# Kernel optimization log

Measured on AMD Instinct MI355X. Metric: run time of the kernel, lower is better.

## Reference

```python
import jax, jax.numpy as jnp
import numpy as np

B, L, D = 16, 4096, 512
WORD_SIZE = 2048  # codebook_size // 4
WORD_LEN = 2


def setup_inputs() -> dict:
    key = jax.random.key(0)
    k1, k2, k3, k4, k5 = jax.random.split(key, 5)
    char_tokens = jax.random.randint(k1, (B, L), 0, 8192, dtype=jnp.int64 if jax.config.jax_enable_x64 else jnp.int32)
    char_embeddings = jax.random.normal(k2, (B, L, D), dtype=jnp.float32)
    # word_codebook initialized uniform(-1/word_size, 1/word_size) in the original
    word_codebook = jax.random.uniform(k3, (WORD_SIZE, D), dtype=jnp.float32,
                                       minval=-1.0 / WORD_SIZE, maxval=1.0 / WORD_SIZE)
    proj_w = jax.random.normal(k4, (D, D), dtype=jnp.float32) * (1.0 / np.sqrt(D))
    proj_b = jax.random.normal(k5, (D,), dtype=jnp.float32) * 0.01
    return {"char_tokens": char_tokens, "char_embeddings": char_embeddings,
            "word_codebook": word_codebook, "proj_w": proj_w, "proj_b": proj_b}


def reference(char_tokens, char_embeddings, word_codebook, proj_w, proj_b):
    Bv, Lv, Dv = char_embeddings.shape
    G = Lv // WORD_LEN  # number of 2-char groups per sequence
    # mean-pool each consecutive pair of characters -> [B, G, D]
    means = char_embeddings.reshape(Bv, G, WORD_LEN, Dv).mean(axis=2)
    # squared-euclidean nearest codebook entry (same argmin as cdist)
    # d2[b,g,k] = ||m||^2 - 2 m.W^T + ||W||^2 ; ||m||^2 constant over k -> drop
    dots = jnp.einsum('bgd,kd->bgk', means, word_codebook)            # [B,G,K]
    cb_sq = jnp.sum(word_codebook * word_codebook, axis=-1)           # [K]
    word_indices = jnp.argmin(cb_sq[None, None, :] - 2.0 * dots, axis=-1)  # [B,G]
    word_embeddings = word_codebook[word_indices]                     # [B,G,D]
    # alignment loss: mse(proj(word_emb), stop_grad(word_emb))
    projected = jnp.einsum('bgd,ed->bge', word_embeddings, proj_w) + proj_b
    target = jax.lax.stop_gradient(word_embeddings)
    alignment_loss = jnp.mean((projected - target) ** 2)
    return (word_indices, word_embeddings, alignment_loss)
```

## Files before the change

### kernel.cpp

```cpp
#include <hip/hip_runtime.h>


#define D_DIM    512
#define K_CODES  2048
#define N_ROWS   32768
#define EPS_GAP  1e-5f
#define LOSS_SCALE (1.0f / 16777216.0f)

typedef __attribute__((ext_vector_type(8))) short short8;
typedef __attribute__((ext_vector_type(4))) float f32x4;

__device__ __forceinline__ void split_bf16(float f, unsigned short& h, unsigned short& l) {
    unsigned u = __float_as_uint(f);
    h = (unsigned short)(u >> 16);
    float hr = __uint_as_float(u & 0xFFFF0000u);
    l = (unsigned short)(__float_as_uint(f - hr) >> 16);
}

__device__ __forceinline__ void dma16(const void* g, void* l) {
    __builtin_amdgcn_global_load_lds(
        (const __attribute__((address_space(1))) unsigned int*)g,
        (__attribute__((address_space(3))) unsigned int*)l, 16, 0, 0);
}

__device__ __forceinline__ void merge_cand(float s, int idx, float& v1, int& i1, float& v2, int& i2) {
    if (s < v1 || (s == v1 && idx < i1)) { v2 = v1; i2 = i1; v1 = s; i1 = idx; }
    else if (s < v2 || (s == v2 && idx < i2)) { v2 = s; i2 = idx; }
}

__global__ __launch_bounds__(256, 1)
void cra_pack_a(const float* __restrict__ ce,
                unsigned short* __restrict__ Ap)
{
    const int tid = threadIdx.x;
    const int mb  = blockIdx.x;
    const int rq  = tid >> 5;
    const int dq  = tid & 31;
    const int dbase = dq * 16;
    const int ach = dq >> 1;
    const int k0  = (dq & 1) * 16;

    #pragma unroll 2
    for (int p = 0; p < 16; ++p) {
        const int r  = p * 8 + rq;
        const int gr = mb * 128 + r;
        const float* a0 = ce + (size_t)(2 * gr) * D_DIM + dbase;
        const float* a1 = a0 + D_DIM;
        float4 x0[4], x1[4];
        #pragma unroll
        for (int q = 0; q < 4; ++q) {
            x0[q] = *(const float4*)(a0 + q * 4);
            x1[q] = *(const float4*)(a1 + q * 4);
        }
        short8 h8[2], l8[2];
        #pragma unroll
        for (int q = 0; q < 4; ++q) {
            const float m[4] = {0.5f * (x0[q].x + x1[q].x), 0.5f * (x0[q].y + x1[q].y),
                                0.5f * (x0[q].z + x1[q].z), 0.5f * (x0[q].w + x1[q].w)};
            #pragma unroll
            for (int e = 0; e < 4; ++e) {
                unsigned short hh, ll;
                split_bf16(m[e], hh, ll);
                h8[q >> 1][(q & 1) * 4 + e] = (short)hh;
                l8[q >> 1][(q & 1) * 4 + e] = (short)ll;
            }
        }
        const size_t hb = ((size_t)(mb * 32 + ach) * 128 + r) * 32 + k0;
        const size_t lb = ((size_t)(mb * 32 + 16 + ach) * 128 + r) * 32 + k0;
        *(short8*)(Ap + hb)     = h8[0];
        *(short8*)(Ap + hb + 8) = h8[1];
        *(short8*)(Ap + lb)     = l8[0];
        *(short8*)(Ap + lb + 8) = l8[1];
    }
}

__global__ __launch_bounds__(256, 1)
void cra_pack_b(const float* __restrict__ cb,
                unsigned short* __restrict__ Bp,
                float* __restrict__ cb_sq,
                float* __restrict__ Sk,
                int* __restrict__ counter,
                float* __restrict__ loss_out)
{
    __shared__ float cbs[32 * D_DIM];
    const int tid = threadIdx.x;
    const int c0  = blockIdx.x * 32;

    if (blockIdx.x == 0) {
        #pragma unroll
        for (int j = 0; j < 8; ++j) Sk[tid + j * 256] = 0.0f;
        if (tid == 0) { counter[0] = 0; loss_out[0] = 0.0f; }
    }

    {
        const float4* src = (const float4*)(cb + (size_t)c0 * D_DIM);
        float4* dst = (float4*)cbs;
        #pragma unroll
        for (int k = 0; k < 16; ++k) dst[tid + k * 256] = src[tid + k * 256];
    }
    __syncthreads();

    if (tid < 32) {
        const float* r = cbs + tid * D_DIM;
        float s = 0.f;
        for (int d = 0; d < D_DIM; ++d) s = fmaf(r[d], r[d], s);
        cb_sq[c0 + tid] = s;
    }

    const int row  = tid >> 3;
    const int k    = c0 + row;
    const int colb = k >> 7;
    const int pr   = k & 127;
    const int dspan = (tid & 7) * 64;
    #pragma unroll
    for (int g = 0; g < 8; ++g) {
        const int d   = dspan + g * 8;
        const int bch = d >> 5;
        const int k0  = d & 31;
        short8 h8, l8;
        #pragma unroll
        for (int e = 0; e < 8; ++e) {
            unsigned short hh, ll;
            split_bf16(cbs[row * D_DIM + d + e], hh, ll);
            h8[e] = (short)hh; l8[e] = (short)ll;
        }
        *(short8*)(Bp + ((size_t)(colb * 32 + bch) * 128 + pr) * 32 + k0)      = h8;
        *(short8*)(Bp + ((size_t)(colb * 32 + 16 + bch) * 128 + pr) * 32 + k0) = l8;
    }
}

__global__ __launch_bounds__(256, 1)
void cra_proj(const float* __restrict__ cb,
              const float* __restrict__ W,
              const float* __restrict__ pb,
              float* __restrict__ Sk)
{
    __shared__ float cbs[32 * D_DIM];
    __shared__ float red[4 * 32];
    const int tid = threadIdx.x;
    const int cblock = blockIdx.x >> 2;
    const int eb     = blockIdx.x & 3;
    const int c0 = cblock * 32;

    {
        const float4* src = (const float4*)(cb + (size_t)c0 * D_DIM);
        float4* dst = (float4*)cbs;
        #pragma unroll
        for (int k = 0; k < 16; ++k) dst[tid + k * 256] = src[tid + k * 256];
    }
    __syncthreads();

    const int e  = eb * 128 + (tid >> 1);
    const int dh = (tid & 1) * 256;
    float acc[32];
    #pragma unroll
    for (int c = 0; c < 32; ++c) acc[c] = 0.f;
    const float4* wrow = (const float4*)(W + (size_t)e * D_DIM + dh);
    for (int dq = 0; dq < 64; ++dq) {
        const float4 wv = wrow[dq];
        #pragma unroll
        for (int c = 0; c < 32; ++c) {
            const float4 cv = *(const float4*)&cbs[c * D_DIM + dh + dq * 4];
            acc[c] += cv.x * wv.x + cv.y * wv.y + cv.z * wv.z + cv.w * wv.w;
        }
    }
    const float bias = pb[e];
    const int w = tid >> 6;
    #pragma unroll
    for (int c = 0; c < 32; ++c) {
        const float full = acc[c] + __shfl_xor(acc[c], 1);
        const float diff = full + bias - cbs[c * D_DIM + e];
        float v = (tid & 1) ? 0.f : diff * diff;
        #pragma unroll
        for (int off = 32; off > 0; off >>= 1) v += __shfl_down(v, off, 64);
        if ((tid & 63) == 0) red[w * 32 + c] = v;
    }
    __syncthreads();
    if (tid < 32)
        atomicAdd(&Sk[c0 + tid],
                  red[tid] + red[32 + tid] + red[64 + tid] + red[96 + tid]);
}

__global__ __launch_bounds__(256, 3)
void cra_gemm(const unsigned short* __restrict__ Ap,
              const unsigned short* __restrict__ Bp,
              const float* __restrict__ cb_sq,
              float4* __restrict__ wsRed)
{
    __shared__ short sMem[8192];
    short* sA = sMem;
    short* sB = sMem + 4096;

    const int tid  = threadIdx.x;
    const int bid  = blockIdx.x;
    const int xcd  = bid & 7;
    const int slot = bid >> 3;
    const int mb   = xcd * 32 + (slot >> 4);
    const int colb = slot & 15;
    const int rowBase = mb * 128;
    const int colBase = colb * 128;

    const int lane = tid & 63;
    const int w    = tid >> 6;
    const int wr   = (w & 1) * 64;
    const int wcH  = w >> 1;
    const int wc   = wcH * 64;
    const int cid  = lane & 15;
    const int quad = lane >> 4;

    f32x4 acc[4][4];
    #pragma unroll
    for (int i = 0; i < 4; ++i)
        #pragma unroll
        for (int j = 0; j < 4; ++j) acc[i][j] = (f32x4)(0.f);

    const char* Ag = (const char*)Ap + ((size_t)mb   * 32) * 8192 + w * 2048 + lane * 16;
    const char* Bg = (const char*)Bp + ((size_t)colb * 32) * 8192 + w * 2048 + lane * 16;
    char* lA = (char*)sA + w * 2048;
    char* lB = (char*)sB + w * 2048;

    #pragma unroll 1
    for (int g = 0; g < 48; ++g) {
        const int ach = g & 31;
        const int bch = (g & 15) | ((g & 32) >> 1);
        const char* ag = Ag + ach * 8192;
        const char* bg = Bg + bch * 8192;
        dma16(ag,        lA);
        dma16(ag + 1024, lA + 1024);
        dma16(bg,        lB);
        dma16(bg + 1024, lB + 1024);
        __syncthreads();

        short8 aF[4], bF[4];
        #pragma unroll
        for (int mi = 0; mi < 4; ++mi) aF[mi] = *(const short8*)&sA[(wr + mi * 16 + cid) * 32 + quad * 8];
        #pragma unroll
        for (int ni = 0; ni < 4; ++ni) bF[ni] = *(const short8*)&sB[(wc + ni * 16 + cid) * 32 + quad * 8];
        #pragma unroll
        for (int mi = 0; mi < 4; ++mi)
            #pragma unroll
            for (int ni = 0; ni < 4; ++ni)
                acc[mi][ni] = __builtin_amdgcn_mfma_f32_16x16x32_bf16(aF[mi], bF[ni], acc[mi][ni], 0, 0, 0);
        __syncthreads();
    }

    float cq[4];
    #pragma unroll
    for (int ni = 0; ni < 4; ++ni) cq[ni] = cb_sq[colBase + wc + ni * 16 + cid];

    float4* sRed = (float4*)sMem;
    #pragma unroll
    for (int mi = 0; mi < 4; ++mi) {
        #pragma unroll
        for (int reg = 0; reg < 4; ++reg) {
            float v1 = 3.4e38f, v2 = 3.4e38f;
            int   i1 = 0x7FFFFFFF, i2 = 0x7FFFFFFF;
            #pragma unroll
            for (int ni = 0; ni < 4; ++ni) {
                const float s = fmaf(-2.0f, acc[mi][ni][reg], cq[ni]);
                merge_cand(s, colBase + wc + ni * 16 + cid, v1, i1, v2, i2);
            }
            #pragma unroll
            for (int d = 1; d <= 2; d <<= 1) {
                float ov1 = __shfl_xor(v1, d); int oi1 = __shfl_xor(i1, d);
                float ov2 = __shfl_xor(v2, d); int oi2 = __shfl_xor(i2, d);
                merge_cand(ov1, oi1, v1, i1, v2, i2);
                merge_cand(ov2, oi2, v1, i1, v2, i2);
            }
            if ((cid & 3) == 0) {
                const int row = wr + mi * 16 + quad * 4 + reg;
                sRed[(row * 2 + wcH) * 4 + (cid >> 2)] =
                    make_float4(v1, __int_as_float(i1), v2, __int_as_float(i2));
            }
        }
    }
    __syncthreads();
    if (tid < 128) {
        float v1 = 3.4e38f, v2 = 3.4e38f;
        int   i1 = 0x7FFFFFFF, i2 = 0x7FFFFFFF;
        #pragma unroll
        for (int e = 0; e < 8; ++e) {
            const float4 t = sRed[tid * 8 + e];
            merge_cand(t.x, __float_as_int(t.y), v1, i1, v2, i2);
            merge_cand(t.z, __float_as_int(t.w), v1, i1, v2, i2);
        }
        wsRed[(size_t)(rowBase + tid) * 16 + colb] =
            make_float4(v1, __int_as_float(i1), v2, __int_as_float(i2));
    }
}

__global__ __launch_bounds__(256, 1)
void cra_merge(const float4* __restrict__ wsRed,
               const float* __restrict__ Sk,
               float* __restrict__ out_idx,
               float* __restrict__ out_loss,
               int* __restrict__ counter,
               int* __restrict__ flagRow,
               int2* __restrict__ flagI)
{
    __shared__ float sl[256];
    const int tid = threadIdx.x;
    const int r = blockIdx.x * 256 + tid;
    float v1 = 3.4e38f, v2 = 3.4e38f;
    int   i1 = 0x7FFFFFFF, i2 = 0x7FFFFFFF;
    #pragma unroll 4
    for (int cbk = 0; cbk < 16; ++cbk) {
        const float4 t = wsRed[(size_t)r * 16 + cbk];
        merge_cand(t.x, __float_as_int(t.y), v1, i1, v2, i2);
        merge_cand(t.z, __float_as_int(t.w), v1, i1, v2, i2);
    }
    out_idx[r] = (float)i1;
    if (v2 - v1 < EPS_GAP) {
        const int slot = atomicAdd(counter, 1);
        flagRow[slot] = r;
        flagI[slot] = make_int2(i1, i2);
    }
    sl[tid] = Sk[i1];
    __syncthreads();
    for (int s = 128; s > 0; s >>= 1) { if (tid < s) sl[tid] += sl[tid + s]; __syncthreads(); }
    if (tid == 0) atomicAdd(out_loss, sl[0] * LOSS_SCALE);
}

__global__ __launch_bounds__(256, 1)
void cra_gather(const float* __restrict__ out_idx,
                const float4* __restrict__ cb4,
                float4* __restrict__ out4)
{
    __shared__ int sidx[128];
    const int tid = threadIdx.x;
    const int rb = blockIdx.x * 128;
    if (tid < 128) sidx[tid] = (int)out_idx[rb + tid];
    __syncthreads();
    for (int j = tid; j < 128 * 128; j += 256) {
        const int row = j >> 7, q = j & 127;
        out4[(size_t)(rb + row) * 128 + q] = cb4[(size_t)sidx[row] * 128 + q];
    }
}

__global__ __launch_bounds__(256, 1)
void cra_recheck(const float* __restrict__ ce,
                 const float* __restrict__ cb,
                 const float* __restrict__ cb_sq,
                 const float* __restrict__ Sk,
                 const int* __restrict__ counter,
                 const int* __restrict__ flagRow,
                 const int2* __restrict__ flagI,
                 float* __restrict__ out_idx,
                 float4* __restrict__ out4,
                 float* __restrict__ out_loss,
                 const float4* __restrict__ cb4)
{
    __shared__ float rp[8];
    __shared__ int swin;
    const int tid = threadIdx.x;
    const int n = counter[0];
    for (int f = blockIdx.x; f < n; f += 64) {
        const int row = flagRow[f];
        const int2 ii = flagI[f];
        const int d0 = tid * 2;
        const float2 x0 = *(const float2*)(ce + (size_t)(2 * row) * D_DIM + d0);
        const float2 x1 = *(const float2*)(ce + (size_t)(2 * row) * D_DIM + D_DIM + d0);
        const float m0 = 0.5f * (x0.x + x1.x), m1 = 0.5f * (x0.y + x1.y);
        const float* c1 = cb + (size_t)ii.x * D_DIM + d0;
        const float* c2 = cb + (size_t)ii.y * D_DIM + d0;
        float p1 = fmaf(m0, c1[0], m1 * c1[1]);
        float p2 = fmaf(m0, c2[0], m1 * c2[1]);
        #pragma unroll
        for (int off = 32; off > 0; off >>= 1) {
            p1 += __shfl_down(p1, off, 64);
            p2 += __shfl_down(p2, off, 64);
        }
        if ((tid & 63) == 0) { rp[(tid >> 6) * 2] = p1; rp[(tid >> 6) * 2 + 1] = p2; }
        __syncthreads();
        if (tid == 0) {
            const float dot1 = rp[0] + rp[2] + rp[4] + rp[6];
            const float dot2 = rp[1] + rp[3] + rp[5] + rp[7];
            const float s1 = cb_sq[ii.x] - 2.f * dot1;
            const float s2 = cb_sq[ii.y] - 2.f * dot2;
            const int win = (s2 < s1 || (s2 == s1 && ii.y < ii.x)) ? ii.y : ii.x;
            swin = win;
            if (win != ii.x) {
                out_idx[row] = (float)win;
                atomicAdd(out_loss, (Sk[win] - Sk[ii.x]) * LOSS_SCALE);
            }
        }
        __syncthreads();
        if (swin != ii.x) {
            for (int q = tid; q < 128; q += 256)
                out4[(size_t)row * 128 + q] = cb4[(size_t)swin * 128 + q];
        }
        __syncthreads();
    }
}

extern "C" void kernel_launch(void* const* d_in, const int* in_sizes, int n_in,
                              void* d_out, int out_size, void* d_ws, size_t ws_size,
                              hipStream_t stream)
{
    const float* ce = (const float*)d_in[1];
    const float* cb = (const float*)d_in[2];
    const float* W  = (const float*)d_in[3];
    const float* pb = (const float*)d_in[4];

    char* ws = (char*)d_ws;
    unsigned short* Bp = (unsigned short*)ws;
    float4* wsRed  = (float4*)(ws + 4194304);
    float* cb_sq   = (float*)(ws + 12582912);
    float* Sk      = (float*)(ws + 12582912 + 8192);
    int*   flagRow = (int*)(ws + 12582912 + 16384);
    int2*  flagI   = (int2*)(ws + 12582912 + 16384 + 131072);
    int*   counter = (int*)(ws + 12582912 + 16384 + 131072 + 262144);

    float* out_idx  = (float*)d_out;
    float* out_emb  = out_idx + N_ROWS;
    float* out_loss = out_emb + (size_t)N_ROWS * D_DIM;
    unsigned short* Ap = (unsigned short*)out_emb;

    cra_pack_a<<<256, 256, 0, stream>>>(ce, Ap);
    cra_pack_b<<<64, 256, 0, stream>>>(cb, Bp, cb_sq, Sk, counter, out_loss);
    cra_proj<<<256, 256, 0, stream>>>(cb, W, pb, Sk);
    cra_gemm<<<4096, 256, 0, stream>>>(Ap, Bp, cb_sq, wsRed);
    cra_merge<<<128, 256, 0, stream>>>(wsRed, Sk, out_idx, out_loss, counter, flagRow, flagI);
    cra_gather<<<256, 256, 0, stream>>>(out_idx, (const float4*)cb, (float4*)out_emb);
    cra_recheck<<<64, 256, 0, stream>>>(ce, cb, cb_sq, Sk, counter, flagRow, flagI,
                                        out_idx, (float4*)out_emb, out_loss, (const float4*)cb);
}
```

Baseline: 867.0 us.

## Rework split-bf16 GEMM into 256x256 tiles with swizzled LDS and double-buffered DMA

Replaces the 128x128, 256-thread GEMM, which syncs twice per 32-wide K step, with a 512-thread 256x256 tile kernel. Each stage loads 64-wide K chunks into a 128KB LDS double buffer through direct global-to-LDS DMA, and explicit vmcnt waits let the next stage's loads overlap the current stage's MFMAs. The pack kernels now write A and B pre-swizzled (XOR pattern) so LDS fragment reads avoid bank conflicts, and the merge stage now combines 8 column partials per row instead of 16. The larger tiles raise data reuse per byte loaded but use much more LDS and registers, which lowers occupancy.

```diff
diff --git a/kernel.cpp b/kernel.cpp
--- a/kernel.cpp
+++ b/kernel.cpp
@@ -10,6 +10,8 @@
 typedef __attribute__((ext_vector_type(8))) short short8;
 typedef __attribute__((ext_vector_type(4))) float f32x4;
 
+#define SWZ(L) ((L) ^ (((L) >> 1) & 0x40) ^ (((L) >> 4) & 0x30))
+
 __device__ __forceinline__ void split_bf16(float f, unsigned short& h, unsigned short& l) {
     unsigned u = __float_as_uint(f);
     h = (unsigned short)(u >> 16);
@@ -32,19 +34,24 @@
 void cra_pack_a(const float* __restrict__ ce,
                 unsigned short* __restrict__ Ap)
 {
-    const int tid = threadIdx.x;
-    const int mb  = blockIdx.x;
-    const int rq  = tid >> 5;
-    const int dq  = tid & 31;
-    const int dbase = dq * 16;
-    const int ach = dq >> 1;
-    const int k0  = (dq & 1) * 16;
+    const int tid   = threadIdx.x;
+    const int mb128 = blockIdx.x;
+    const int mb256 = mb128 >> 1;
+    const int half  = mb128 & 1;
+    const int rq = tid >> 5;
+    const int dq = tid & 31;
+    const int d0 = dq * 16;
+    const int j  = dq >> 2;
+    const int k0 = (dq & 3) * 16;
+
+    const size_t hbase = ((size_t)((mb256 * 16 + j) * 2 + half)) * 8192;
+    const size_t lbase = ((size_t)((mb256 * 16 + 8 + j) * 2 + half)) * 8192;
 
     #pragma unroll 2
     for (int p = 0; p < 16; ++p) {
         const int r  = p * 8 + rq;
-        const int gr = mb * 128 + r;
-        const float* a0 = ce + (size_t)(2 * gr) * D_DIM + dbase;
+        const int gr = mb128 * 128 + r;
+        const float* a0 = ce + (size_t)(2 * gr) * D_DIM + d0;
         const float* a1 = a0 + D_DIM;
         float4 x0[4], x1[4];
         #pragma unroll
@@ -65,12 +72,13 @@
                 l8[q >> 1][(q & 1) * 4 + e] = (short)ll;
             }
         }
-        const size_t hb = ((size_t)(mb * 32 + ach) * 128 + r) * 32 + k0;
-        const size_t lb = ((size_t)(mb * 32 + 16 + ach) * 128 + r) * 32 + k0;
-        *(short8*)(Ap + hb)     = h8[0];
-        *(short8*)(Ap + hb + 8) = h8[1];
-        *(short8*)(Ap + lb)     = l8[0];
-        *(short8*)(Ap + lb + 8) = l8[1];
+        const int L1 = r * 128 + k0 * 2;
+        const int S1 = SWZ(L1);
+        const int S2 = SWZ(L1 + 16);
+        *(short8*)(Ap + hbase + (S1 >> 1)) = h8[0];
+        *(short8*)(Ap + hbase + (S2 >> 1)) = h8[1];
+        *(short8*)(Ap + lbase + (S1 >> 1)) = l8[0];
+        *(short8*)(Ap + lbase + (S2 >> 1)) = l8[1];
     }
 }
 
@@ -107,16 +115,18 @@
         cb_sq[c0 + tid] = s;
     }
 
-    const int row  = tid >> 3;
-    const int k    = c0 + row;
-    const int colb = k >> 7;
-    const int pr   = k & 127;
+    const int row   = tid >> 3;
+    const int k     = c0 + row;
+    const int colb  = k >> 8;
+    const int cc    = k & 255;
+    const int halfB = cc >> 7;
+    const int rB    = cc & 127;
     const int dspan = (tid & 7) * 64;
     #pragma unroll
     for (int g = 0; g < 8; ++g) {
-        const int d   = dspan + g * 8;
-        const int bch = d >> 5;
-        const int k0  = d & 31;
+        const int d  = dspan + g * 8;
+        const int j  = d >> 6;
+        const int kk = d & 63;
         short8 h8, l8;
         #pragma unroll
         for (int e = 0; e < 8; ++e) {
@@ -124,8 +134,9 @@
             split_bf16(cbs[row * D_DIM + d + e], hh, ll);
             h8[e] = (short)hh; l8[e] = (short)ll;
         }
-        *(short8*)(Bp + ((size_t)(colb * 32 + bch) * 128 + pr) * 32 + k0)      = h8;
-        *(short8*)(Bp + ((size_t)(colb * 32 + 16 + bch) * 128 + pr) * 32 + k0) = l8;
+        const int S = SWZ(rB * 128 + kk * 2);
+        *(short8*)(Bp + ((size_t)((colb * 16 + j) * 2 + halfB)) * 8192 + (S >> 1))     = h8;
+        *(short8*)(Bp + ((size_t)((colb * 16 + 8 + j) * 2 + halfB)) * 8192 + (S >> 1)) = l8;
     }
 }
 
@@ -181,76 +192,109 @@
                   red[tid] + red[32 + tid] + red[64 + tid] + red[96 + tid]);
 }
 
-__global__ __launch_bounds__(256, 3)
+__global__ __launch_bounds__(512, 2)
 void cra_gemm(const unsigned short* __restrict__ Ap,
               const unsigned short* __restrict__ Bp,
               const float* __restrict__ cb_sq,
               float4* __restrict__ wsRed)
 {
-    __shared__ short sMem[8192];
-    short* sA = sMem;
-    short* sB = sMem + 4096;
+    __shared__ __align__(16) char sMem[131072];
 
     const int tid  = threadIdx.x;
     const int bid  = blockIdx.x;
-    const int xcd  = bid & 7;
-    const int slot = bid >> 3;
-    const int mb   = xcd * 32 + (slot >> 4);
-    const int colb = slot & 15;
-    const int rowBase = mb * 128;
-    const int colBase = colb * 128;
+    const int wgid = (bid & 7) * 128 + (bid >> 3);
+    const int mb   = wgid >> 3;
+    const int colb = wgid & 7;
+    const int rowBase = mb * 256;
+    const int colBase = colb * 256;
 
     const int lane = tid & 63;
     const int w    = tid >> 6;
-    const int wr   = (w & 1) * 64;
-    const int wcH  = w >> 1;
-    const int wc   = wcH * 64;
+    const int wm   = w >> 2;
+    const int wn   = w & 3;
     const int cid  = lane & 15;
     const int quad = lane >> 4;
 
-    f32x4 acc[4][4];
-    #pragma unroll
-    for (int i = 0; i < 4; ++i)
-        #pragma unroll
-        for (int j = 0; j < 4; ++j) acc[i][j] = (f32x4)(0.f);
-
-    const char* Ag = (const char*)Ap + ((size_t)mb   * 32) * 8192 + w * 2048 + lane * 16;
-    const char* Bg = (const char*)Bp + ((size_t)colb * 32) * 8192 + w * 2048 + lane * 16;
-    char* lA = (char*)sA + w * 2048;
-    char* lB = (char*)sB + w * 2048;
+    const int swzm = ((cid & 1) << 6) | (((cid >> 1) & 3) << 4);
+    const int aRT  = (cid * 128 + quad * 16) ^ swzm;
+    const int bRT  = ((((wn & 1) * 64 + cid) * 128) + quad * 16) ^ swzm;
+
+    const char* AgBase = (const char*)Ap + (size_t)(mb * 16) * 32768 + w * 1024 + lane * 16;
+    const char* BgBase = (const char*)Bp + (size_t)(colb * 16) * 32768 + w * 1024 + lane * 16;
+
+    f32x4 acc[8][4];
+    #pragma unroll
+    for (int mi = 0; mi < 8; ++mi)
+        #pragma unroll
+        for (int ni = 0; ni < 4; ++ni) acc[mi][ni] = (f32x4)(0.f);
+
+    #pragma unroll
+    for (int p = 0; p < 2; ++p) {
+        const char* ag = AgBase + (size_t)p * 32768;
+        const char* bg = BgBase + (size_t)p * 32768;
+        char* la = sMem + p * 65536 + w * 1024;
+        char* lb = la + 32768;
+        #pragma unroll
+        for (int jj = 0; jj < 4; ++jj) {
+            dma16(ag + jj * 8192, la + jj * 8192);
+            dma16(bg + jj * 8192, lb + jj * 8192);
+        }
+    }
 
     #pragma unroll 1
-    for (int g = 0; g < 48; ++g) {
-        const int ach = g & 31;
-        const int bch = (g & 15) | ((g & 32) >> 1);
-        const char* ag = Ag + ach * 8192;
-        const char* bg = Bg + bch * 8192;
-        dma16(ag,        lA);
-        dma16(ag + 1024, lA + 1024);
-        dma16(bg,        lB);
-        dma16(bg + 1024, lB + 1024);
-        __syncthreads();
-
-        short8 aF[4], bF[4];
-        #pragma unroll
-        for (int mi = 0; mi < 4; ++mi) aF[mi] = *(const short8*)&sA[(wr + mi * 16 + cid) * 32 + quad * 8];
-        #pragma unroll
-        for (int ni = 0; ni < 4; ++ni) bF[ni] = *(const short8*)&sB[(wc + ni * 16 + cid) * 32 + quad * 8];
-        #pragma unroll
-        for (int mi = 0; mi < 4; ++mi)
+    for (int t = 0; t < 24; ++t) {
+        const int p = t & 1;
+        if (t < 23) asm volatile("s_waitcnt vmcnt(8)\n\ts_barrier" ::: "memory");
+        else        asm volatile("s_waitcnt vmcnt(0)\n\ts_barrier" ::: "memory");
+
+        const char* sAh = sMem + p * 65536 + wm * 16384;
+        const char* sBh = sMem + p * 65536 + 32768 + (wn >> 1) * 16384;
+
+        #pragma unroll
+        for (int ks = 0; ks < 2; ++ks) {
+            short8 af[8], bf[4];
+            #pragma unroll
+            for (int mi = 0; mi < 8; ++mi)
+                af[mi] = *(const short8*)(sAh + ((aRT ^ (ks << 6)) + mi * 2048));
             #pragma unroll
             for (int ni = 0; ni < 4; ++ni)
-                acc[mi][ni] = __builtin_amdgcn_mfma_f32_16x16x32_bf16(aF[mi], bF[ni], acc[mi][ni], 0, 0, 0);
-        __syncthreads();
-    }
+                bf[ni] = *(const short8*)(sBh + ((bRT ^ (ks << 6)) + ni * 2048));
+            __builtin_amdgcn_s_setprio(1);
+            #pragma unroll
+            for (int mi = 0; mi < 8; ++mi)
+                #pragma unroll
+                for (int ni = 0; ni < 4; ++ni)
+                    acc[mi][ni] = __builtin_amdgcn_mfma_f32_16x16x32_bf16(af[mi], bf[ni], acc[mi][ni], 0, 0, 0);
+            __builtin_amdgcn_s_setprio(0);
+        }
+
+        asm volatile("s_waitcnt lgkmcnt(0)\n\ts_barrier" ::: "memory");
+
+        if (t + 2 < 24) {
+            const int tn = t + 2;
+            const int at = tn < 16 ? tn : tn - 16;
+            const int bt = tn < 8 ? tn : tn - 8;
+            const char* ag = AgBase + (size_t)at * 32768;
+            const char* bg = BgBase + (size_t)bt * 32768;
+            char* la = sMem + p * 65536 + w * 1024;
+            char* lb = la + 32768;
+            #pragma unroll
+            for (int jj = 0; jj < 4; ++jj) {
+                dma16(ag + jj * 8192, la + jj * 8192);
+                dma16(bg + jj * 8192, lb + jj * 8192);
+            }
+        }
+    }
+
+    __syncthreads();
+    float4* sRed = (float4*)sMem;
 
     float cq[4];
     #pragma unroll
-    for (int ni = 0; ni < 4; ++ni) cq[ni] = cb_sq[colBase + wc + ni * 16 + cid];
-
-    float4* sRed = (float4*)sMem;
-    #pragma unroll
-    for (int mi = 0; mi < 4; ++mi) {
+    for (int ni = 0; ni < 4; ++ni) cq[ni] = cb_sq[colBase + wn * 64 + ni * 16 + cid];
+
+    #pragma unroll
+    for (int mi = 0; mi < 8; ++mi) {
         #pragma unroll
         for (int reg = 0; reg < 4; ++reg) {
             float v1 = 3.4e38f, v2 = 3.4e38f;
@@ -258,7 +302,7 @@
             #pragma unroll
             for (int ni = 0; ni < 4; ++ni) {
                 const float s = fmaf(-2.0f, acc[mi][ni][reg], cq[ni]);
-                merge_cand(s, colBase + wc + ni * 16 + cid, v1, i1, v2, i2);
+                merge_cand(s, colBase + wn * 64 + ni * 16 + cid, v1, i1, v2, i2);
             }
             #pragma unroll
             for (int d = 1; d <= 2; d <<= 1) {
@@ -268,23 +312,23 @@
                 merge_cand(ov2, oi2, v1, i1, v2, i2);
             }
             if ((cid & 3) == 0) {
-                const int row = wr + mi * 16 + quad * 4 + reg;
-                sRed[(row * 2 + wcH) * 4 + (cid >> 2)] =
+                const int rl = wm * 128 + mi * 16 + quad * 4 + reg;
+                sRed[(rl * 4 + wn) * 4 + (cid >> 2)] =
                     make_float4(v1, __int_as_float(i1), v2, __int_as_float(i2));
             }
         }
     }
     __syncthreads();
-    if (tid < 128) {
+    if (tid < 256) {
         float v1 = 3.4e38f, v2 = 3.4e38f;
         int   i1 = 0x7FFFFFFF, i2 = 0x7FFFFFFF;
         #pragma unroll
-        for (int e = 0; e < 8; ++e) {
-            const float4 t = sRed[tid * 8 + e];
-            merge_cand(t.x, __float_as_int(t.y), v1, i1, v2, i2);
-            merge_cand(t.z, __float_as_int(t.w), v1, i1, v2, i2);
-        }
-        wsRed[(size_t)(rowBase + tid) * 16 + colb] =
+        for (int e = 0; e < 16; ++e) {
+            const float4 q = sRed[tid * 16 + e];
+            merge_cand(q.x, __float_as_int(q.y), v1, i1, v2, i2);
+            merge_cand(q.z, __float_as_int(q.w), v1, i1, v2, i2);
+        }
+        wsRed[(size_t)(rowBase + tid) * 8 + colb] =
             make_float4(v1, __int_as_float(i1), v2, __int_as_float(i2));
     }
 }
@@ -304,8 +348,8 @@
     float v1 = 3.4e38f, v2 = 3.4e38f;
     int   i1 = 0x7FFFFFFF, i2 = 0x7FFFFFFF;
     #pragma unroll 4
-    for (int cbk = 0; cbk < 16; ++cbk) {
-        const float4 t = wsRed[(size_t)r * 16 + cbk];
+    for (int cbk = 0; cbk < 8; ++cbk) {
+        const float4 t = wsRed[(size_t)r * 8 + cbk];
         merge_cand(t.x, __float_as_int(t.y), v1, i1, v2, i2);
         merge_cand(t.z, __float_as_int(t.w), v1, i1, v2, i2);
     }
@@ -419,7 +463,7 @@
     cra_pack_a<<<256, 256, 0, stream>>>(ce, Ap);
     cra_pack_b<<<64, 256, 0, stream>>>(cb, Bp, cb_sq, Sk, counter, out_loss);
     cra_proj<<<256, 256, 0, stream>>>(cb, W, pb, Sk);
-    cra_gemm<<<4096, 256, 0, stream>>>(Ap, Bp, cb_sq, wsRed);
+    cra_gemm<<<1024, 512, 0, stream>>>(Ap, Bp, cb_sq, wsRed);
     cra_merge<<<128, 256, 0, stream>>>(wsRed, Sk, out_idx, out_loss, counter, flagRow, flagI);
     cra_gather<<<256, 256, 0, stream>>>(out_idx, (const float4*)cb, (float4*)out_emb);
     cra_recheck<<<64, 256, 0, stream>>>(ce, cb, cb_sq, Sk, counter, flagRow, flagI,
```

After: 975.1 us. +12.5%, slower.

## Load GEMM fragments directly from global into registers with double buffering

Applied to the files above, without the earlier changes.

Drops the LDS staging of A/B tiles through global_load_lds and the two barriers per k-step in the distance GEMM. Each wave now loads its MFMA fragments straight from the pre-packed global buffers into registers, using two register sets so the next step's loads overlap the current MFMAs, and raises wave priority around the MFMA block. The trade-off is that data shared between waves is no longer reused through LDS, so global/L2 traffic per block roughly doubles, and the extra fragment registers may hurt occupancy.

```diff
diff --git a/kernel.cpp b/kernel.cpp
--- a/kernel.cpp
+++ b/kernel.cpp
@@ -15,12 +15,6 @@
     h = (unsigned short)(u >> 16);
     float hr = __uint_as_float(u & 0xFFFF0000u);
     l = (unsigned short)(__float_as_uint(f - hr) >> 16);
-}
-
-__device__ __forceinline__ void dma16(const void* g, void* l) {
-    __builtin_amdgcn_global_load_lds(
-        (const __attribute__((address_space(1))) unsigned int*)g,
-        (__attribute__((address_space(3))) unsigned int*)l, 16, 0, 0);
 }
 
 __device__ __forceinline__ void merge_cand(float s, int idx, float& v1, int& i1, float& v2, int& i2) {
@@ -187,9 +181,7 @@
               const float* __restrict__ cb_sq,
               float4* __restrict__ wsRed)
 {
-    __shared__ short sMem[8192];
-    short* sA = sMem;
-    short* sB = sMem + 4096;
+    __shared__ float4 sRed[128 * 8];
 
     const int tid  = threadIdx.x;
     const int bid  = blockIdx.x;
@@ -214,41 +206,47 @@
         #pragma unroll
         for (int j = 0; j < 4; ++j) acc[i][j] = (f32x4)(0.f);
 
-    const char* Ag = (const char*)Ap + ((size_t)mb   * 32) * 8192 + w * 2048 + lane * 16;
-    const char* Bg = (const char*)Bp + ((size_t)colb * 32) * 8192 + w * 2048 + lane * 16;
-    char* lA = (char*)sA + w * 2048;
-    char* lB = (char*)sB + w * 2048;
-
+    const unsigned short* Abase = Ap + ((size_t)mb   * 32) * 4096 + (wr + cid) * 32 + quad * 8;
+    const unsigned short* Bbase = Bp + ((size_t)colb * 32) * 4096 + (wc + cid) * 32 + quad * 8;
+
+#define LOADF(af, bf, g) do {                                                  \
+        const int ach_ = (g) & 31;                                             \
+        const int bch_ = ((g) & 15) | (((g) & 32) >> 1);                       \
+        const unsigned short* pa_ = Abase + ach_ * 4096;                       \
+        const unsigned short* pb_ = Bbase + bch_ * 4096;                       \
+        af[0] = *(const short8*)(pa_);        af[1] = *(const short8*)(pa_ + 512);  \
+        af[2] = *(const short8*)(pa_ + 1024); af[3] = *(const short8*)(pa_ + 1536); \
+        bf[0] = *(const short8*)(pb_);        bf[1] = *(const short8*)(pb_ + 512);  \
+        bf[2] = *(const short8*)(pb_ + 1024); bf[3] = *(const short8*)(pb_ + 1536); \
+    } while (0)
+
+#define DOMFMA(af, bf) do {                                                    \
+        __builtin_amdgcn_s_setprio(1);                                         \
+        _Pragma("unroll")                                                      \
+        for (int mi = 0; mi < 4; ++mi)                                         \
+            _Pragma("unroll")                                                  \
+            for (int ni = 0; ni < 4; ++ni)                                     \
+                acc[mi][ni] = __builtin_amdgcn_mfma_f32_16x16x32_bf16(         \
+                    af[mi], bf[ni], acc[mi][ni], 0, 0, 0);                     \
+        __builtin_amdgcn_s_setprio(0);                                         \
+    } while (0)
+
+    short8 afA[4], bfA[4], afB[4], bfB[4];
+    LOADF(afA, bfA, 0);
     #pragma unroll 1
-    for (int g = 0; g < 48; ++g) {
-        const int ach = g & 31;
-        const int bch = (g & 15) | ((g & 32) >> 1);
-        const char* ag = Ag + ach * 8192;
-        const char* bg = Bg + bch * 8192;
-        dma16(ag,        lA);
-        dma16(ag + 1024, lA + 1024);
-        dma16(bg,        lB);
-        dma16(bg + 1024, lB + 1024);
-        __syncthreads();
-
-        short8 aF[4], bF[4];
-        #pragma unroll
-        for (int mi = 0; mi < 4; ++mi) aF[mi] = *(const short8*)&sA[(wr + mi * 16 + cid) * 32 + quad * 8];
-        #pragma unroll
-        for (int ni = 0; ni < 4; ++ni) bF[ni] = *(const short8*)&sB[(wc + ni * 16 + cid) * 32 + quad * 8];
-        #pragma unroll
-        for (int mi = 0; mi < 4; ++mi)
-            #pragma unroll
-            for (int ni = 0; ni < 4; ++ni)
-                acc[mi][ni] = __builtin_amdgcn_mfma_f32_16x16x32_bf16(aF[mi], bF[ni], acc[mi][ni], 0, 0, 0);
-        __syncthreads();
-    }
+    for (int g = 0; g < 48; g += 2) {
+        LOADF(afB, bfB, g + 1);
+        DOMFMA(afA, bfA);
+        if (g + 2 < 48) LOADF(afA, bfA, g + 2);
+        DOMFMA(afB, bfB);
+    }
+#undef LOADF
+#undef DOMFMA
 
     float cq[4];
     #pragma unroll
     for (int ni = 0; ni < 4; ++ni) cq[ni] = cb_sq[colBase + wc + ni * 16 + cid];
 
-    float4* sRed = (float4*)sMem;
     #pragma unroll
     for (int mi = 0; mi < 4; ++mi) {
         #pragma unroll
```

Result: slower. 1.057 ms (+21.9%).
